# Kernel tuning notes

Measured on AMD Instinct MI355X. Metric: run time of the kernel, lower is better.

## Reference

```python
import jax, jax.numpy as jnp
import numpy as np

BETA = 0.2        # RPE learning rate (init kwarg, unused in forward output math except P update)
THRESH = 0.5      # BrainCog IFNode default firing threshold; v starts at 0 -> spike = (x >= THRESH)
N_NEURONS = 33554432


def setup_inputs() -> dict:
    key = jax.random.key(0)
    spikes = jax.random.uniform(key, (N_NEURONS,), dtype=jnp.float32)
    P = jnp.zeros((N_NEURONS,), dtype=jnp.float32)  # reward prediction state
    return {"spikes": spikes, "P": P}


def reference(spikes, P):
    # Vectorized IF neurons: membrane v = 0 + spikes; fire if v >= threshold (hard reset).
    out_spikes = (spikes >= THRESH).astype(spikes.dtype)   # [n_neurons]
    S = out_spikes.mean()                                  # scalar mean firing rate
    delta = S - P                                          # [n_neurons] reward prediction error
    # (State update in original: P <- P + BETA * delta; forward returns (delta, out_spikes).)
    return (delta, out_spikes)
```

## Files before the change

kernel.cpp:

```cpp
#include <hip/hip_runtime.h>


#define THRESH 0.5f
#define BLOCK  256
#define GRID   2048

typedef float v4f __attribute__((ext_vector_type(4)));

__device__ __forceinline__ int spike4(const v4f s, v4f& o) {
    o.x = (s.x >= THRESH) ? 1.0f : 0.0f;
    o.y = (s.y >= THRESH) ? 1.0f : 0.0f;
    o.z = (s.z >= THRESH) ? 1.0f : 0.0f;
    o.w = (s.w >= THRESH) ? 1.0f : 0.0f;
    return (int)o.x + (int)o.y + (int)o.z + (int)o.w;
}

__global__ __launch_bounds__(BLOCK) void spike_count_kernel(
    const v4f* __restrict__ spikes4,
    v4f* __restrict__ out_spikes4,
    unsigned int* __restrict__ partials,
    int n4, int chunk)
{
    const int tid   = threadIdx.x;
    const int start = blockIdx.x * chunk;
    const int end   = min(start + chunk, n4);
    int cnt = 0;

    int i = start + tid;
    for (; i + 3 * BLOCK < end; i += 4 * BLOCK) {
        v4f a = spikes4[i];
        v4f b = spikes4[i +     BLOCK];
        v4f c = spikes4[i + 2 * BLOCK];
        v4f d = spikes4[i + 3 * BLOCK];
        v4f oa, ob, oc, od;
        cnt += spike4(a, oa);
        cnt += spike4(b, ob);
        cnt += spike4(c, oc);
        cnt += spike4(d, od);
        out_spikes4[i]             = oa;
        out_spikes4[i +     BLOCK] = ob;
        out_spikes4[i + 2 * BLOCK] = oc;
        out_spikes4[i + 3 * BLOCK] = od;
    }
    for (; i < end; i += BLOCK) {
        v4f s = spikes4[i];
        v4f o;
        cnt += spike4(s, o);
        out_spikes4[i] = o;
    }

    #pragma unroll
    for (int off = 32; off > 0; off >>= 1)
        cnt += __shfl_down(cnt, off, 64);

    __shared__ int wave_sums[BLOCK / 64];
    const int lane = tid & 63;
    const int wid  = tid >> 6;
    if (lane == 0) wave_sums[wid] = cnt;
    __syncthreads();
    if (tid == 0) {
        int total = 0;
        #pragma unroll
        for (int w = 0; w < BLOCK / 64; ++w) total += wave_sums[w];
        partials[blockIdx.x] = (unsigned int)total;
    }
}

__global__ __launch_bounds__(BLOCK) void delta_kernel(
    const v4f* __restrict__ P4,
    v4f* __restrict__ delta4,
    const unsigned int* __restrict__ partials,
    int n_part, int n4, int chunk, float inv_n)
{
    const int tid = threadIdx.x;

    int c = 0;
    for (int j = tid; j < n_part; j += BLOCK)
        c += (int)partials[j];
    #pragma unroll
    for (int off = 32; off > 0; off >>= 1)
        c += __shfl_down(c, off, 64);

    __shared__ int wave_sums[BLOCK / 64];
    const int lane = tid & 63;
    const int wid  = tid >> 6;
    if (lane == 0) wave_sums[wid] = c;
    __syncthreads();
    int total = 0;
    #pragma unroll
    for (int w = 0; w < BLOCK / 64; ++w) total += wave_sums[w];
    const float S = (float)total * inv_n;

    const int start = blockIdx.x * chunk;
    const int end   = min(start + chunk, n4);
    int i = start + tid;
    for (; i + 3 * BLOCK < end; i += 4 * BLOCK) {
        v4f a  = P4[i];
        v4f b  = P4[i +     BLOCK];
        v4f c4 = P4[i + 2 * BLOCK];
        v4f d  = P4[i + 3 * BLOCK];
        delta4[i]             = S - a;
        delta4[i +     BLOCK] = S - b;
        delta4[i + 2 * BLOCK] = S - c4;
        delta4[i + 3 * BLOCK] = S - d;
    }
    for (; i < end; i += BLOCK) {
        v4f p = P4[i];
        delta4[i] = S - p;
    }
}

extern "C" void kernel_launch(void* const* d_in, const int* in_sizes, int n_in,
                              void* d_out, int out_size, void* d_ws, size_t ws_size,
                              hipStream_t stream) {
    const float* spikes = (const float*)d_in[0];
    const float* P      = (const float*)d_in[1];
    float* out          = (float*)d_out;

    const int n  = in_sizes[0];
    const int n4 = n / 4;
    const int chunk = (n4 + GRID - 1) / GRID;
    float* delta_out  = out;
    float* spikes_out = out + n;

    unsigned int* partials = (unsigned int*)d_ws;

    spike_count_kernel<<<GRID, BLOCK, 0, stream>>>(
        (const v4f*)spikes, (v4f*)spikes_out, partials, n4, chunk);

    delta_kernel<<<GRID, BLOCK, 0, stream>>>(
        (const v4f*)P, (v4f*)delta_out, partials, GRID, n4, chunk,
        1.0f / (float)n);
}
```

Measured before the change: 432.9 us.

## Fuse count and delta kernels with a grid-wide atomic barrier

Merges the spike-count and delta kernels into one persistent launch. Blocks publish partial counts, then spin on an atomic arrival counter before each block sums all partials and writes delta. This removes the second kernel launch and its tail/ramp gap, and halves the grid so that all blocks can be co-resident for the barrier. It adds a hipMemsetAsync and relies on every block being resident at once, with the risk of deadlock if they are not. It also assumes n4 divides evenly by the grid.

Measured after the change: 565.1 us. 1.31x slower.

```diff
diff --git a/kernel.cpp b/kernel.cpp
--- a/kernel.cpp
+++ b/kernel.cpp
@@ -3,7 +3,7 @@
 
 #define THRESH 0.5f
 #define BLOCK  256
-#define GRID   2048
+#define GRID   1024
 
 typedef float v4f __attribute__((ext_vector_type(4)));
 
@@ -15,17 +15,22 @@
     return (int)o.x + (int)o.y + (int)o.z + (int)o.w;
 }
 
-__global__ __launch_bounds__(BLOCK) void spike_count_kernel(
+__global__ __launch_bounds__(BLOCK) void fused_kernel(
     const v4f* __restrict__ spikes4,
+    const v4f* __restrict__ P4,
     v4f* __restrict__ out_spikes4,
-    unsigned int* __restrict__ partials,
-    int n4, int chunk)
+    v4f* __restrict__ delta4,
+    unsigned int* ws,
+    int chunk, float inv_n)
 {
+    unsigned int* arrive   = ws;
+    unsigned int* partials = ws + 64;
+
     const int tid   = threadIdx.x;
     const int start = blockIdx.x * chunk;
-    const int end   = min(start + chunk, n4);
+    const int end   = start + chunk;
+
     int cnt = 0;
-
     int i = start + tid;
     for (; i + 3 * BLOCK < end; i += 4 * BLOCK) {
         v4f a = spikes4[i];
@@ -52,48 +57,34 @@
     #pragma unroll
     for (int off = 32; off > 0; off >>= 1)
         cnt += __shfl_down(cnt, off, 64);
+    __shared__ int wave_sums[BLOCK / 64];
+    if ((tid & 63) == 0) wave_sums[tid >> 6] = cnt;
+    __syncthreads();
 
-    __shared__ int wave_sums[BLOCK / 64];
-    const int lane = tid & 63;
-    const int wid  = tid >> 6;
-    if (lane == 0) wave_sums[wid] = cnt;
+    if (tid == 0) {
+        int total = wave_sums[0] + wave_sums[1] + wave_sums[2] + wave_sums[3];
+        atomicExch(&partials[blockIdx.x], (unsigned int)total);
+        __threadfence();
+        atomicAdd(arrive, 1u);
+        while (atomicAdd(arrive, 0u) < (unsigned int)gridDim.x)
+            __builtin_amdgcn_s_sleep(2);
+    }
     __syncthreads();
-    if (tid == 0) {
-        int total = 0;
-        #pragma unroll
-        for (int w = 0; w < BLOCK / 64; ++w) total += wave_sums[w];
-        partials[blockIdx.x] = (unsigned int)total;
-    }
-}
-
-__global__ __launch_bounds__(BLOCK) void delta_kernel(
-    const v4f* __restrict__ P4,
-    v4f* __restrict__ delta4,
-    const unsigned int* __restrict__ partials,
-    int n_part, int n4, int chunk, float inv_n)
-{
-    const int tid = threadIdx.x;
 
     int c = 0;
-    for (int j = tid; j < n_part; j += BLOCK)
-        c += (int)partials[j];
+    for (int j = tid; j < GRID; j += BLOCK)
+        c += (int)__hip_atomic_load(&partials[j], __ATOMIC_RELAXED,
+                                    __HIP_MEMORY_SCOPE_AGENT);
     #pragma unroll
     for (int off = 32; off > 0; off >>= 1)
         c += __shfl_down(c, off, 64);
-
-    __shared__ int wave_sums[BLOCK / 64];
-    const int lane = tid & 63;
-    const int wid  = tid >> 6;
-    if (lane == 0) wave_sums[wid] = c;
+    __shared__ int wave_sums2[BLOCK / 64];
+    if ((tid & 63) == 0) wave_sums2[tid >> 6] = c;
     __syncthreads();
-    int total = 0;
-    #pragma unroll
-    for (int w = 0; w < BLOCK / 64; ++w) total += wave_sums[w];
+    const int total = wave_sums2[0] + wave_sums2[1] + wave_sums2[2] + wave_sums2[3];
     const float S = (float)total * inv_n;
 
-    const int start = blockIdx.x * chunk;
-    const int end   = min(start + chunk, n4);
-    int i = start + tid;
+    i = start + tid;
     for (; i + 3 * BLOCK < end; i += 4 * BLOCK) {
         v4f a  = P4[i];
         v4f b  = P4[i +     BLOCK];
@@ -119,16 +110,16 @@
 
     const int n  = in_sizes[0];
     const int n4 = n / 4;
-    const int chunk = (n4 + GRID - 1) / GRID;
+    const int chunk = n4 / GRID;
+
     float* delta_out  = out;
     float* spikes_out = out + n;
+    unsigned int* ws  = (unsigned int*)d_ws;
 
-    unsigned int* partials = (unsigned int*)d_ws;
+    hipMemsetAsync(ws, 0, sizeof(unsigned int), stream);
 
-    spike_count_kernel<<<GRID, BLOCK, 0, stream>>>(
-        (const v4f*)spikes, (v4f*)spikes_out, partials, n4, chunk);
-
-    delta_kernel<<<GRID, BLOCK, 0, stream>>>(
-        (const v4f*)P, (v4f*)delta_out, partials, GRID, n4, chunk,
-        1.0f / (float)n);
+    fused_kernel<<<GRID, BLOCK, 0, stream>>>(
+        (const v4f*)spikes, (const v4f*)P,
+        (v4f*)spikes_out, (v4f*)delta_out,
+        ws, chunk, 1.0f / (float)n);
 }
```

## Split spike counting from spike map and use grid-stride loops with smaller grid

Applied to the files above, without the earlier changes.

Separates the fused threshold-and-count pass into a read-only count kernel and a separate map kernel that writes the spike output, and switches all kernels from per-block contiguous chunks to grid-stride loops over a 512-block grid. The intent is a cleaner streaming access pattern and a pure-read reduction pass. In exchange, the spikes input is read twice and an extra launch is added, and tail handling is dropped, assuming n4 is a multiple of the block stride.

Result: no change. 440.3 us (+1.7%).

```diff
diff --git a/kernel.cpp b/kernel.cpp
--- a/kernel.cpp
+++ b/kernel.cpp
@@ -3,7 +3,8 @@
 
 #define THRESH 0.5f
 #define BLOCK  256
-#define GRID   2048
+#define GRID   512
+#define STEP   (GRID * BLOCK * 4)
 
 typedef float v4f __attribute__((ext_vector_type(4)));
 
@@ -15,54 +16,53 @@
     return (int)o.x + (int)o.y + (int)o.z + (int)o.w;
 }
 
-__global__ __launch_bounds__(BLOCK) void spike_count_kernel(
-    const v4f* __restrict__ spikes4,
-    v4f* __restrict__ out_spikes4,
+__global__ __launch_bounds__(BLOCK) void count_kernel(
+    const v4f* __restrict__ in,
     unsigned int* __restrict__ partials,
-    int n4, int chunk)
+    int n4)
 {
-    const int tid   = threadIdx.x;
-    const int start = blockIdx.x * chunk;
-    const int end   = min(start + chunk, n4);
+    const int tid = threadIdx.x;
     int cnt = 0;
-
-    int i = start + tid;
-    for (; i + 3 * BLOCK < end; i += 4 * BLOCK) {
-        v4f a = spikes4[i];
-        v4f b = spikes4[i +     BLOCK];
-        v4f c = spikes4[i + 2 * BLOCK];
-        v4f d = spikes4[i + 3 * BLOCK];
-        v4f oa, ob, oc, od;
-        cnt += spike4(a, oa);
-        cnt += spike4(b, ob);
-        cnt += spike4(c, oc);
-        cnt += spike4(d, od);
-        out_spikes4[i]             = oa;
-        out_spikes4[i +     BLOCK] = ob;
-        out_spikes4[i + 2 * BLOCK] = oc;
-        out_spikes4[i + 3 * BLOCK] = od;
-    }
-    for (; i < end; i += BLOCK) {
-        v4f s = spikes4[i];
-        v4f o;
-        cnt += spike4(s, o);
-        out_spikes4[i] = o;
+    int i = blockIdx.x * (BLOCK * 4) + tid;
+    for (; i + 3 * BLOCK < n4; i += STEP) {
+        v4f a = in[i];
+        v4f b = in[i +     BLOCK];
+        v4f c = in[i + 2 * BLOCK];
+        v4f d = in[i + 3 * BLOCK];
+        v4f t;
+        cnt += spike4(a, t); cnt += spike4(b, t);
+        cnt += spike4(c, t); cnt += spike4(d, t);
     }
 
     #pragma unroll
     for (int off = 32; off > 0; off >>= 1)
         cnt += __shfl_down(cnt, off, 64);
+    __shared__ int wave_sums[BLOCK / 64];
+    if ((tid & 63) == 0) wave_sums[tid >> 6] = cnt;
+    __syncthreads();
+    if (tid == 0)
+        partials[blockIdx.x] = (unsigned int)(wave_sums[0] + wave_sums[1] +
+                                              wave_sums[2] + wave_sums[3]);
+}
 
-    __shared__ int wave_sums[BLOCK / 64];
-    const int lane = tid & 63;
-    const int wid  = tid >> 6;
-    if (lane == 0) wave_sums[wid] = cnt;
-    __syncthreads();
-    if (tid == 0) {
-        int total = 0;
-        #pragma unroll
-        for (int w = 0; w < BLOCK / 64; ++w) total += wave_sums[w];
-        partials[blockIdx.x] = (unsigned int)total;
+__global__ __launch_bounds__(BLOCK) void map_kernel(
+    const v4f* __restrict__ in,
+    v4f* __restrict__ outv,
+    int n4)
+{
+    const int tid = threadIdx.x;
+    int i = blockIdx.x * (BLOCK * 4) + tid;
+    for (; i + 3 * BLOCK < n4; i += STEP) {
+        v4f a = in[i];
+        v4f b = in[i +     BLOCK];
+        v4f c = in[i + 2 * BLOCK];
+        v4f d = in[i + 3 * BLOCK];
+        v4f oa, ob, oc, od;
+        spike4(a, oa); spike4(b, ob); spike4(c, oc); spike4(d, od);
+        outv[i]             = oa;
+        outv[i +     BLOCK] = ob;
+        outv[i + 2 * BLOCK] = oc;
+        outv[i + 3 * BLOCK] = od;
     }
 }
 
@@ -70,43 +70,30 @@
     const v4f* __restrict__ P4,
     v4f* __restrict__ delta4,
     const unsigned int* __restrict__ partials,
-    int n_part, int n4, int chunk, float inv_n)
+    int n4, float inv_n)
 {
     const int tid = threadIdx.x;
 
-    int c = 0;
-    for (int j = tid; j < n_part; j += BLOCK)
-        c += (int)partials[j];
+    int c = (int)partials[tid] + (int)partials[tid + BLOCK];
     #pragma unroll
     for (int off = 32; off > 0; off >>= 1)
         c += __shfl_down(c, off, 64);
-
     __shared__ int wave_sums[BLOCK / 64];
-    const int lane = tid & 63;
-    const int wid  = tid >> 6;
-    if (lane == 0) wave_sums[wid] = c;
+    if ((tid & 63) == 0) wave_sums[tid >> 6] = c;
     __syncthreads();
-    int total = 0;
-    #pragma unroll
-    for (int w = 0; w < BLOCK / 64; ++w) total += wave_sums[w];
+    const int total = wave_sums[0] + wave_sums[1] + wave_sums[2] + wave_sums[3];
     const float S = (float)total * inv_n;
 
-    const int start = blockIdx.x * chunk;
-    const int end   = min(start + chunk, n4);
-    int i = start + tid;
-    for (; i + 3 * BLOCK < end; i += 4 * BLOCK) {
-        v4f a  = P4[i];
-        v4f b  = P4[i +     BLOCK];
+    int i = blockIdx.x * (BLOCK * 4) + tid;
+    for (; i + 3 * BLOCK < n4; i += STEP) {
+        v4f a = P4[i];
+        v4f b = P4[i +     BLOCK];
         v4f c4 = P4[i + 2 * BLOCK];
-        v4f d  = P4[i + 3 * BLOCK];
+        v4f d = P4[i + 3 * BLOCK];
         delta4[i]             = S - a;
         delta4[i +     BLOCK] = S - b;
         delta4[i + 2 * BLOCK] = S - c4;
         delta4[i + 3 * BLOCK] = S - d;
-    }
-    for (; i < end; i += BLOCK) {
-        v4f p = P4[i];
-        delta4[i] = S - p;
     }
 }
 
@@ -119,16 +106,17 @@
 
     const int n  = in_sizes[0];
     const int n4 = n / 4;
-    const int chunk = (n4 + GRID - 1) / GRID;
     float* delta_out  = out;
     float* spikes_out = out + n;
 
     unsigned int* partials = (unsigned int*)d_ws;
 
-    spike_count_kernel<<<GRID, BLOCK, 0, stream>>>(
-        (const v4f*)spikes, (v4f*)spikes_out, partials, n4, chunk);
+    count_kernel<<<GRID, BLOCK, 0, stream>>>(
+        (const v4f*)spikes, partials, n4);
+
+    map_kernel<<<GRID, BLOCK, 0, stream>>>(
+        (const v4f*)spikes, (v4f*)spikes_out, n4);
 
     delta_kernel<<<GRID, BLOCK, 0, stream>>>(
-        (const v4f*)P, (v4f*)delta_out, partials, GRID, n4, chunk,
-        1.0f / (float)n);
+        (const v4f*)P, (v4f*)delta_out, partials, n4, 1.0f / (float)n);
 }
```
